# Kernel optimization log

Measured on AMD Instinct MI355X. Metric: run time of the kernel, lower is better.

## Reference

```python
import jax, jax.numpy as jnp
import numpy as np

B, T, V, H, L = 2048, 128, 256, 20, 15  # batch, seq_len, vocab, hidden, max_label


def setup_inputs() -> dict:
    key = jax.random.key(0)
    ks = jax.random.split(key, 8)
    g = lambda k, shape, s: (jax.random.normal(k, shape, jnp.float32) * s)
    return {
        "x": jax.random.randint(ks[0], (B, T), 0, V, dtype=jnp.int32),
        "W0": g(ks[1], (V, 3 * H), 0.06),   # input kernel layer 0 [V, 3H] (z|r|h)
        "U0": g(ks[2], (H, 3 * H), 0.2),    # recurrent kernel layer 0
        "b0i": jnp.zeros((3 * H,), jnp.float32),  # input bias (reset_after=True split bias)
        "b0r": jnp.zeros((3 * H,), jnp.float32),  # recurrent bias
        "W1": g(ks[3], (H, 3 * H), 0.2),
        "U1": g(ks[4], (H, 3 * H), 0.2),
        "b1i": jnp.zeros((3 * H,), jnp.float32),
        "b1r": jnp.zeros((3 * H,), jnp.float32),
        "Wd": g(ks[5], (H, L), 0.2),
        "bd": jnp.zeros((L,), jnp.float32),
        "drop_rate": 0,  # identity dropout (deterministic reference)
    }


def _gru_cell(h, xw, U, br):
    # Keras GRUCell with reset_after=True:
    #   xw = x @ W + b_in  (precomputed), rec = h @ U + b_rec
    rec = h @ U + br
    xz, xr, xh = jnp.split(xw, 3, axis=-1)
    rz, rr, rh = jnp.split(rec, 3, axis=-1)
    z = jax.nn.sigmoid(xz + rz)
    r = jax.nn.sigmoid(xr + rr)
    hh = jnp.tanh(xh + r * rh)
    return z * h + (1.0 - z) * hh


def reference(x, W0, U0, b0i, b0r, W1, U1, b1i, b1r, Wd, bd, drop_rate):
    # one_hot(x) @ W0 == gather rows of W0 (same math, no [B,T,V] materialization)
    xW0 = W0[x] + b0i                 # [B, T, 3H]
    xW0 = jnp.swapaxes(xW0, 0, 1)     # [T, B, 3H] for scan over time

    def step(carry, xw_t):
        h0, h1 = carry
        h0 = _gru_cell(h0, xw_t, U0, b0r)
        xw1 = h0 @ W1 + b1i
        h1 = _gru_cell(h1, xw1, U1, b1r)
        return (h0, h1), None

    h0 = jnp.zeros((x.shape[0], H), W0.dtype)
    h1 = jnp.zeros((x.shape[0], H), W0.dtype)
    (h0, h1), _ = jax.lax.scan(step, (h0, h1), xW0)
    # tf.nn.dropout with rate 0 is the identity
    out = h1
    logits = jax.nn.softmax(out @ Wd + bd, axis=-1)  # [B, L]
    return logits
```

## Files before the change

### kernel.cpp

```cpp
#include <hip/hip_runtime.h>


#define BB 2048
#define TT 128
#define HH 20
#define LL 15
#define H3 60

typedef float v2f __attribute__((ext_vector_type(2)));

__device__ __forceinline__ float bclane(float v, int k) {
    return __int_as_float(__builtin_amdgcn_readlane(__float_as_int(v), k));
}
__device__ __forceinline__ float dpp_rshr1(float v) {
    return __int_as_float(__builtin_amdgcn_update_dpp(
        0, __float_as_int(v), 0x111, 0xF, 0xF, true));
}
__device__ __forceinline__ float fast_rcp(float x) { return __builtin_amdgcn_rcpf(x); }
__device__ __forceinline__ float sigm(float x) { return fast_rcp(1.f + __expf(-x)); }
__device__ __forceinline__ float tanh_f(float x) { return 1.f - 2.f * fast_rcp(1.f + __expf(2.f * x)); }
#define PIN(v) asm volatile("" : "+v"(v))
#define LDSFENCE() asm volatile("" ::: "memory")

extern "C" __global__ __launch_bounds__(512)
__attribute__((amdgpu_waves_per_eu(4, 4)))
void gru2_kernel(const int* __restrict__ x, const float* __restrict__ W0,
                 const float* __restrict__ U0, const float* __restrict__ b0i,
                 const float* __restrict__ b0r, const float* __restrict__ W1,
                 const float* __restrict__ U1, const float* __restrict__ b1i,
                 const float* __restrict__ b1r, const float* __restrict__ Wd,
                 const float* __restrict__ bd, float* __restrict__ out)
{
    const int lane = threadIdx.x & 63;
    const int wv = threadIdx.x >> 6;
    const bool isL1 = (wv >= 4);
    const int wb = wv & 3;
    const int b = blockIdx.x * 4 + wb;

    const int pos = lane & 15;
    const int pc  = (pos < 15) ? pos : 14;
    const int u   = pc / 3;
    const int p3  = pc % 3;
    const int j   = (lane >> 4) * 5 + u;
    const bool home = (pos < 15) && (p3 == 2);
    const int col = p3 * 20 + j;

    __shared__ __align__(16) float h0x[4][2][24];
    __shared__ __align__(16) float h1s[4][24];
    if (home) { h0x[wb][0][j] = 0.f; h0x[wb][1][j] = 0.f; h1s[wb][j] = 0.f; }
    __syncthreads();

    const float* MA = isL1 ? W1 : U0;
    const float* MB = isL1 ? U1 : U0;
    v2f wA[10], wB[10];
#pragma unroll
    for (int q = 0; q < 10; ++q) {
        const int k0 = (2 * q) * H3, k1 = (2 * q + 1) * H3;
        wA[q] = v2f{MA[k0 + col], MA[k1 + col]};
        wB[q] = v2f{MB[k0 + col], MB[k1 + col]};
    }
#pragma unroll
    for (int q = 0; q < 10; ++q) { PIN(wA[q]); PIN(wB[q]); }
    const float dbA = isL1 ? b1i[col] : b0r[col];
    const float dbB = isL1 ? b1r[col] : 0.f;
    const float bi0c = b0i[col];

    const int* xrow = x + b * TT;
    int tokA = 0, tokB = 0, tokn2 = 0;
    float xw_cur = 0.f, xw_nxt = 0.f;
    if (!isL1) {
        tokA = xrow[lane];
        tokB = xrow[64 + lane];
        const int tok0 = __builtin_amdgcn_readlane(tokA, 0);
        const int tok1 = __builtin_amdgcn_readlane(tokA, 1);
        tokn2 = __builtin_amdgcn_readlane(tokA, 2);
        xw_cur = W0[tok0 * H3 + col] + bi0c;
        xw_nxt = W0[tok1 * H3 + col];
    }

    float h0 = 0.f, h1 = 0.f;

    for (int i = 0; i <= TT; ++i) {
        if (!isL1) {
            if (i < TT) {
                const int t3 = (i + 3 < TT) ? (i + 3) : (TT - 1);
                const float pf = W0[tokn2 * H3 + col];
                const int tokn3 =
                    __builtin_amdgcn_readlane(t3 < 64 ? tokA : tokB, t3 & 63);

                const float4* hq = (const float4*)&h0x[wb][(i + 1) & 1][0];
                v2f a0 = v2f{dbA, 0.f};
#pragma unroll
                for (int q = 0; q < 5; ++q) {
                    const float4 hv = hq[q];
                    a0 = __builtin_elementwise_fma(v2f{hv.x, hv.y}, wA[2 * q], a0);
                    a0 = __builtin_elementwise_fma(v2f{hv.z, hv.w}, wA[2 * q + 1], a0);
                }
                const float rec0 = a0.x + a0.y;

                const float sg0 = sigm(xw_cur + rec0);
                const float rv0 = dpp_rshr1(sg0);
                const float zv0 = dpp_rshr1(rv0);
                const float hh0 = tanh_f(xw_cur + rv0 * rec0);
                h0 = fmaf(zv0, h0 - hh0, hh0);
                if (home) h0x[wb][i & 1][j] = h0;
                LDSFENCE();

                xw_cur = xw_nxt + bi0c; xw_nxt = pf; tokn2 = tokn3;
            }
        } else {
            if (i >= 1) {
                const float4* hq = (const float4*)&h0x[wb][(i + 1) & 1][0];
                const float4* gq = (const float4*)&h1s[wb][0];
                v2f a1 = v2f{dbA, 0.f}, a2 = v2f{dbB, 0.f};
#pragma unroll
                for (int q = 0; q < 5; ++q) {
                    const float4 hv = hq[q];
                    const float4 gv = gq[q];
                    a1 = __builtin_elementwise_fma(v2f{hv.x, hv.y}, wA[2 * q], a1);
                    a1 = __builtin_elementwise_fma(v2f{hv.z, hv.w}, wA[2 * q + 1], a1);
                    a2 = __builtin_elementwise_fma(v2f{gv.x, gv.y}, wB[2 * q], a2);
                    a2 = __builtin_elementwise_fma(v2f{gv.z, gv.w}, wB[2 * q + 1], a2);
                }
                const float xw1 = a1.x + a1.y;
                const float rec1 = a2.x + a2.y;

                const float sg1 = sigm(xw1 + rec1);
                const float rv1 = dpp_rshr1(sg1);
                const float zv1 = dpp_rshr1(rv1);
                const float hh1 = tanh_f(xw1 + rv1 * rec1);
                h1 = fmaf(zv1, h1 - hh1, hh1);
                if (home) h1s[wb][j] = h1;
                LDSFENCE();
            }
        }
        __syncthreads();
    }

    if (isL1) {
        const int l = lane < LL ? lane : LL - 1;
        float acc = bd[l];
#pragma unroll
        for (int k = 0; k < HH; ++k)
            acc = fmaf(h1s[wb][k], Wd[k * LL + l], acc);

        float m = acc;
#pragma unroll
        for (int i = 0; i < LL; ++i) m = fmaxf(m, bclane(acc, i));
        const float e = __expf(acc - m);
        float s = 0.f;
#pragma unroll
        for (int i = 0; i < LL; ++i) s += bclane(e, i);
        const float pr = e * fast_rcp(s);

        if (lane < LL) out[b * LL + lane] = pr;
    }
}

extern "C" void kernel_launch(void* const* d_in, const int* in_sizes, int n_in,
                              void* d_out, int out_size, void* d_ws, size_t ws_size,
                              hipStream_t stream) {
    const int*   x   = (const int*)  d_in[0];
    const float* W0  = (const float*)d_in[1];
    const float* U0  = (const float*)d_in[2];
    const float* b0i = (const float*)d_in[3];
    const float* b0r = (const float*)d_in[4];
    const float* W1  = (const float*)d_in[5];
    const float* U1  = (const float*)d_in[6];
    const float* b1i = (const float*)d_in[7];
    const float* b1r = (const float*)d_in[8];
    const float* Wd  = (const float*)d_in[9];
    const float* bd  = (const float*)d_in[10];
    float* out = (float*)d_out;

    dim3 grid(BB / 4), block(512);
    hipLaunchKernelGGL(gru2_kernel, grid, block, 0, stream,
                       x, W0, U0, b0i, b0r, W1, U1, b1i, b1r, Wd, bd, out);
}
```

Before: 140.8 us.

## Shrink blocks to one batch row per workgroup and split FMA accumulator chains

Each workgroup now handles a single batch element with two waves, one per GRU layer, instead of four elements with eight waves. The per-step __syncthreads therefore couples only two waves, which cuts barrier wait caused by skew between unrelated batch rows. The U1 weight registers are loaded only on the layer-1 wave, and the dot-product accumulators are split into two independent chains to shorten the FMA dependency. The cost is four times as many small workgroups, with more per-block setup, while the waves_per_eu hint stays the same.

```diff
diff --git a/kernel.cpp b/kernel.cpp
--- a/kernel.cpp
+++ b/kernel.cpp
@@ -22,7 +22,7 @@
 #define PIN(v) asm volatile("" : "+v"(v))
 #define LDSFENCE() asm volatile("" ::: "memory")
 
-extern "C" __global__ __launch_bounds__(512)
+extern "C" __global__ __launch_bounds__(128)
 __attribute__((amdgpu_waves_per_eu(4, 4)))
 void gru2_kernel(const int* __restrict__ x, const float* __restrict__ W0,
                  const float* __restrict__ U0, const float* __restrict__ b0i,
@@ -32,10 +32,8 @@
                  const float* __restrict__ bd, float* __restrict__ out)
 {
     const int lane = threadIdx.x & 63;
-    const int wv = threadIdx.x >> 6;
-    const bool isL1 = (wv >= 4);
-    const int wb = wv & 3;
-    const int b = blockIdx.x * 4 + wb;
+    const bool isL1 = (threadIdx.x >= 64);
+    const int b = blockIdx.x;
 
     const int pos = lane & 15;
     const int pc  = (pos < 15) ? pos : 14;
@@ -45,22 +43,30 @@
     const bool home = (pos < 15) && (p3 == 2);
     const int col = p3 * 20 + j;
 
-    __shared__ __align__(16) float h0x[4][2][24];
-    __shared__ __align__(16) float h1s[4][24];
-    if (home) { h0x[wb][0][j] = 0.f; h0x[wb][1][j] = 0.f; h1s[wb][j] = 0.f; }
+    __shared__ __align__(16) float h0x[2][24];
+    __shared__ __align__(16) float h1s[24];
+    if (!isL1 && home) { h0x[0][j] = 0.f; h0x[1][j] = 0.f; }
+    if (isL1 && home)  { h1s[j] = 0.f; }
     __syncthreads();
 
     const float* MA = isL1 ? W1 : U0;
-    const float* MB = isL1 ? U1 : U0;
     v2f wA[10], wB[10];
 #pragma unroll
     for (int q = 0; q < 10; ++q) {
         const int k0 = (2 * q) * H3, k1 = (2 * q + 1) * H3;
         wA[q] = v2f{MA[k0 + col], MA[k1 + col]};
-        wB[q] = v2f{MB[k0 + col], MB[k1 + col]};
     }
 #pragma unroll
-    for (int q = 0; q < 10; ++q) { PIN(wA[q]); PIN(wB[q]); }
+    for (int q = 0; q < 10; ++q) PIN(wA[q]);
+    if (isL1) {
+#pragma unroll
+        for (int q = 0; q < 10; ++q) {
+            const int k0 = (2 * q) * H3, k1 = (2 * q + 1) * H3;
+            wB[q] = v2f{U1[k0 + col], U1[k1 + col]};
+        }
+#pragma unroll
+        for (int q = 0; q < 10; ++q) PIN(wB[q]);
+    }
     const float dbA = isL1 ? b1i[col] : b0r[col];
     const float dbB = isL1 ? b1r[col] : 0.f;
     const float bi0c = b0i[col];
@@ -71,11 +77,9 @@
     if (!isL1) {
         tokA = xrow[lane];
         tokB = xrow[64 + lane];
-        const int tok0 = __builtin_amdgcn_readlane(tokA, 0);
-        const int tok1 = __builtin_amdgcn_readlane(tokA, 1);
         tokn2 = __builtin_amdgcn_readlane(tokA, 2);
-        xw_cur = W0[tok0 * H3 + col] + bi0c;
-        xw_nxt = W0[tok1 * H3 + col];
+        xw_cur = W0[__builtin_amdgcn_readlane(tokA, 0) * H3 + col] + bi0c;
+        xw_nxt = W0[__builtin_amdgcn_readlane(tokA, 1) * H3 + col];
     }
 
     float h0 = 0.f, h1 = 0.f;
@@ -88,49 +92,50 @@
                 const int tokn3 =
                     __builtin_amdgcn_readlane(t3 < 64 ? tokA : tokB, t3 & 63);
 
-                const float4* hq = (const float4*)&h0x[wb][(i + 1) & 1][0];
-                v2f a0 = v2f{dbA, 0.f};
+                const float4* hq = (const float4*)&h0x[(i + 1) & 1][0];
+                v2f a0 = v2f{dbA, 0.f}, a0b = v2f{0.f, 0.f};
 #pragma unroll
                 for (int q = 0; q < 5; ++q) {
                     const float4 hv = hq[q];
-                    a0 = __builtin_elementwise_fma(v2f{hv.x, hv.y}, wA[2 * q], a0);
-                    a0 = __builtin_elementwise_fma(v2f{hv.z, hv.w}, wA[2 * q + 1], a0);
+                    a0  = __builtin_elementwise_fma(v2f{hv.x, hv.y}, wA[2 * q], a0);
+                    a0b = __builtin_elementwise_fma(v2f{hv.z, hv.w}, wA[2 * q + 1], a0b);
                 }
-                const float rec0 = a0.x + a0.y;
+                const float rec0 = (a0.x + a0.y) + (a0b.x + a0b.y);
 
                 const float sg0 = sigm(xw_cur + rec0);
                 const float rv0 = dpp_rshr1(sg0);
                 const float zv0 = dpp_rshr1(rv0);
                 const float hh0 = tanh_f(xw_cur + rv0 * rec0);
                 h0 = fmaf(zv0, h0 - hh0, hh0);
-                if (home) h0x[wb][i & 1][j] = h0;
+                if (home) h0x[i & 1][j] = h0;
                 LDSFENCE();
 
                 xw_cur = xw_nxt + bi0c; xw_nxt = pf; tokn2 = tokn3;
             }
         } else {
             if (i >= 1) {
-                const float4* hq = (const float4*)&h0x[wb][(i + 1) & 1][0];
-                const float4* gq = (const float4*)&h1s[wb][0];
-                v2f a1 = v2f{dbA, 0.f}, a2 = v2f{dbB, 0.f};
+                const float4* hq = (const float4*)&h0x[(i + 1) & 1][0];
+                const float4* gq = (const float4*)&h1s[0];
+                v2f a1 = v2f{dbA, 0.f}, a1b = v2f{0.f, 0.f};
+                v2f a2 = v2f{dbB, 0.f}, a2b = v2f{0.f, 0.f};
 #pragma unroll
                 for (int q = 0; q < 5; ++q) {
                     const float4 hv = hq[q];
                     const float4 gv = gq[q];
-                    a1 = __builtin_elementwise_fma(v2f{hv.x, hv.y}, wA[2 * q], a1);
-                    a1 = __builtin_elementwise_fma(v2f{hv.z, hv.w}, wA[2 * q + 1], a1);
-                    a2 = __builtin_elementwise_fma(v2f{gv.x, gv.y}, wB[2 * q], a2);
-                    a2 = __builtin_elementwise_fma(v2f{gv.z, gv.w}, wB[2 * q + 1], a2);
+                    a1  = __builtin_elementwise_fma(v2f{hv.x, hv.y}, wA[2 * q], a1);
+                    a1b = __builtin_elementwise_fma(v2f{hv.z, hv.w}, wA[2 * q + 1], a1b);
+                    a2  = __builtin_elementwise_fma(v2f{gv.x, gv.y}, wB[2 * q], a2);
+                    a2b = __builtin_elementwise_fma(v2f{gv.z, gv.w}, wB[2 * q + 1], a2b);
                 }
-                const float xw1 = a1.x + a1.y;
-                const float rec1 = a2.x + a2.y;
+                const float xw1  = (a1.x + a1.y) + (a1b.x + a1b.y);
+                const float rec1 = (a2.x + a2.y) + (a2b.x + a2b.y);
 
                 const float sg1 = sigm(xw1 + rec1);
                 const float rv1 = dpp_rshr1(sg1);
                 const float zv1 = dpp_rshr1(rv1);
                 const float hh1 = tanh_f(xw1 + rv1 * rec1);
                 h1 = fmaf(zv1, h1 - hh1, hh1);
-                if (home) h1s[wb][j] = h1;
+                if (home) h1s[j] = h1;
                 LDSFENCE();
             }
         }
@@ -142,7 +147,7 @@
         float acc = bd[l];
 #pragma unroll
         for (int k = 0; k < HH; ++k)
-            acc = fmaf(h1s[wb][k], Wd[k * LL + l], acc);
+            acc = fmaf(h1s[k], Wd[k * LL + l], acc);
 
         float m = acc;
 #pragma unroll
@@ -173,7 +178,7 @@
     const float* bd  = (const float*)d_in[10];
     float* out = (float*)d_out;
 
-    dim3 grid(BB / 4), block(512);
+    dim3 grid(BB), block(128);
     hipLaunchKernelGGL(gru2_kernel, grid, block, 0, stream,
                        x, W0, U0, b0i, b0r, W1, U1, b1i, b1r, Wd, bd, out);
 }
```

Result: faster. 133.1 us (-5.5%).
